# Kernel optimization log

Hardware: AMD Instinct MI355X
Metric: run time of the kernel (lower is better)

The kernel has to match this reference:

```python
import jax, jax.numpy as jnp
import numpy as np

N, MEM_SIZE, MEM_DIM = 65536, 2048, 256

def setup_inputs() -> dict:
    key = jax.random.key(0)
    k1, k2 = jax.random.split(key)
    x = jax.random.normal(k1, (N, MEM_DIM), dtype=jnp.float32)
    # xavier_uniform for memory parameter [memory_size, memory_dim]
    limit = np.sqrt(6.0 / (MEM_SIZE + MEM_DIM)).astype(np.float32)
    memory = jax.random.uniform(k2, (MEM_SIZE, MEM_DIM), dtype=jnp.float32,
                                minval=-limit, maxval=limit)
    return {"x": x, "memory": memory}

def reference(x, memory):
    # scores: [N, memory_size] = x @ memory^T (unscaled)
    scores = jnp.einsum('nd,md->nm', x, memory)
    attention_weights = jax.nn.softmax(scores, axis=-1)
    memory_output = jnp.einsum('nm,md->nd', attention_weights, memory)
    return (memory_output, attention_weights)
```

## Files before the change

### kernel.cpp

```cpp
#include <hip/hip_runtime.h>
#include <hip/hip_bf16.h>
#include <stdint.h>

#define NQ 65536
#define MM 2048
#define DD 256

typedef __bf16 bf16x8 __attribute__((ext_vector_type(8)));
typedef float f32x16 __attribute__((ext_vector_type(16)));
typedef unsigned short u16;
typedef unsigned int u32;
typedef u16 u16x8 __attribute__((ext_vector_type(8)));

typedef __attribute__((address_space(3))) u32 lds_u32;
typedef __attribute__((address_space(1))) u32 glb_u32;

#define GLOAD16(gsrc, ldst)                                                    \
  __builtin_amdgcn_global_load_lds((glb_u32*)(uintptr_t)(gsrc),                \
                                   (lds_u32*)(u32)(uintptr_t)(ldst), 16, 0, 0)

__device__ __forceinline__ u16 f32_to_bf16_rtne(float v) {
  u32 u = __builtin_bit_cast(u32, v);
  u += 0x7FFFu + ((u >> 16) & 1u);
  return (u16)(u >> 16);
}

__global__ __launch_bounds__(256) void mem_convert_kernel(
    const float* __restrict__ memory, u16* __restrict__ memb,
    u16* __restrict__ memTswz) {
  int tid = blockIdx.x * 256 + threadIdx.x;
  u16 b = f32_to_bf16_rtne(memory[tid]);
  memb[tid] = b;
  int m = tid >> 8, d = tid & 255;
  int t = m >> 5, mi = m & 31;
  int c = mi >> 3, e = mi & 7;
  int slot = c ^ ((d >> 1) & 3);
  memTswz[(size_t)t * 8192 + (size_t)(d * 4 + slot) * 8 + e] = b;
}

template <bool STORE_BF16>
__global__ __launch_bounds__(256, 2) void pass1_kernel(
    const float* __restrict__ x, const u16* __restrict__ memb,
    u16* __restrict__ p_e, float* __restrict__ outWf,
    float* __restrict__ sums) {
  __shared__ __align__(16) char stage[2][32768];

  const int tid = threadIdx.x;
  const int wv = tid >> 6;
  const int l = tid & 63;
  const int q5 = l & 31;
  const int h = l >> 5;
  const int qw = blockIdx.x * 128 + wv * 32;

  bf16x8 aq[16];
  {
    const float* xrow = x + (size_t)(qw + q5) * DD;
#pragma unroll
    for (int ks = 0; ks < 16; ++ks) {
      const float4 f0 = *(const float4*)(xrow + ks * 16 + h * 8);
      const float4 f1 = *(const float4*)(xrow + ks * 16 + h * 8 + 4);
      bf16x8 a;
      a[0] = (__bf16)f0.x; a[1] = (__bf16)f0.y;
      a[2] = (__bf16)f0.z; a[3] = (__bf16)f0.w;
      a[4] = (__bf16)f1.x; a[5] = (__bf16)f1.y;
      a[6] = (__bf16)f1.z; a[7] = (__bf16)f1.w;
      aq[ks] = a;
    }
  }

  auto STAGE1 = [&](int mt, char* buf) {
#pragma unroll
    for (int i = 0; i < 8; ++i) {
      const int wc = wv * 8 + i;
      const int row = wc * 2 + h;
      const int csrc = q5 ^ (row & 7);
      GLOAD16(memb + (((size_t)(mt * 64 + row)) << 8) + csrc * 8,
              buf + (wc << 10));
    }
  };

  float part[16];
#pragma unroll
  for (int r = 0; r < 16; ++r) part[r] = 0.f;

  STAGE1(0, stage[0]);
  __syncthreads();
  for (int mt = 0; mt < 32; ++mt) {
    char* cur = stage[mt & 1];
    char* nxt = stage[(mt & 1) ^ 1];
    if (mt + 1 < 32) STAGE1(mt + 1, nxt);
#pragma unroll
    for (int msub = 0; msub < 2; ++msub) {
      const int mrow = msub * 32 + q5;
      const char* bbase = cur + mrow * 512;
      const int sw = mrow & 7;
      f32x16 acc = 0.f;
      __builtin_amdgcn_s_setprio(1);
#pragma unroll
      for (int ks = 0; ks < 16; ++ks) {
        bf16x8 b = *(const bf16x8*)(bbase + (((ks * 2 + h) ^ sw) << 4));
        acc = __builtin_amdgcn_mfma_f32_32x32x16_bf16(aq[ks], b, acc, 0, 0, 0);
      }
      __builtin_amdgcn_s_setprio(0);
      const int tm = mt * 2 + msub;
#pragma unroll
      for (int r = 0; r < 16; ++r) {
        const int qrow = (r & 3) + 8 * (r >> 2) + 4 * h;
        const float e = __expf(acc[r]);
        part[r] += e;
        if (STORE_BF16) {
          p_e[(size_t)(qw + qrow) * MM + tm * 32 + q5] = f32_to_bf16_rtne(e);
        } else {
          outWf[(size_t)(qw + qrow) * MM + tm * 32 + q5] = e;
        }
      }
    }
    __syncthreads();
  }

#pragma unroll
  for (int r = 0; r < 16; ++r) {
    float p = part[r];
    p += __shfl_xor(p, 1, 64);
    p += __shfl_xor(p, 2, 64);
    p += __shfl_xor(p, 4, 64);
    p += __shfl_xor(p, 8, 64);
    p += __shfl_xor(p, 16, 64);
    if (q5 == 0) sums[qw + (r & 3) + 8 * (r >> 2) + 4 * h] = p;
  }
}

template <bool LOAD_BF16>
__global__ __launch_bounds__(256, 2) void pass2_kernel(
    const u16* __restrict__ p_e, const u16* __restrict__ memTswz,
    const float* __restrict__ sums, float* __restrict__ outO,
    float* __restrict__ outW) {
  __shared__ __align__(16) char tstage[2][16384];

  const int tid = threadIdx.x;
  const int wv = tid >> 6;
  const int l = tid & 63;
  const int q5 = l & 31;
  const int h = l >> 5;
  const int qw = blockIdx.x * 128 + wv * 32;

  const float inv_lane = 1.0f / sums[qw + q5];
  float invr[16];
#pragma unroll
  for (int r = 0; r < 16; ++r) {
    invr[r] = __shfl(inv_lane, (r & 3) + 8 * (r >> 2) + 4 * h, 64);
  }

  auto STAGE = [&](int t, char* buf) {
#pragma unroll
    for (int i = 0; i < 4; ++i) {
      const int ci = wv * 4 + i;
      GLOAD16(memTswz + ((size_t)t * 1024 + ci * 64 + l) * 8, buf + (ci << 10));
    }
  };

  f32x16 oacc[8];
#pragma unroll
  for (int i = 0; i < 8; ++i) oacc[i] = 0.f;

  STAGE(0, tstage[0]);
  __syncthreads();
  for (int tm = 0; tm < 64; ++tm) {
    char* cur = tstage[tm & 1];
    char* nxt = tstage[(tm & 1) ^ 1];
    if (tm + 1 < 64) STAGE(tm + 1, nxt);

    bf16x8 pa[2];
    if (LOAD_BF16) {
      const u16* prow = p_e + (size_t)(qw + q5) * MM + tm * 32;
#pragma unroll
      for (int ks2 = 0; ks2 < 2; ++ks2) {
        u16x8 pe = *(const u16x8*)(prow + ks2 * 16 + h * 8);
        pa[ks2] = __builtin_bit_cast(bf16x8, pe);
        float w[8];
#pragma unroll
        for (int j = 0; j < 8; ++j) {
          w[j] = __builtin_bit_cast(float, (u32)pe[j] << 16) * inv_lane;
        }
        float* base =
            outW + (size_t)(qw + q5) * MM + tm * 32 + ks2 * 16 + h * 8;
        *(float4*)base = make_float4(w[0], w[1], w[2], w[3]);
        *(float4*)(base + 4) = make_float4(w[4], w[5], w[6], w[7]);
      }
    } else {
      float* wrow = outW + (size_t)(qw + q5) * MM + tm * 32;
#pragma unroll
      for (int ks2 = 0; ks2 < 2; ++ks2) {
        float4 f0 = *(const float4*)(wrow + ks2 * 16 + h * 8);
        float4 f1 = *(const float4*)(wrow + ks2 * 16 + h * 8 + 4);
        float w0 = f0.x * inv_lane, w1 = f0.y * inv_lane;
        float w2 = f0.z * inv_lane, w3 = f0.w * inv_lane;
        float w4 = f1.x * inv_lane, w5 = f1.y * inv_lane;
        float w6 = f1.z * inv_lane, w7 = f1.w * inv_lane;
        *(float4*)(wrow + ks2 * 16 + h * 8) = make_float4(w0, w1, w2, w3);
        *(float4*)(wrow + ks2 * 16 + h * 8 + 4) = make_float4(w4, w5, w6, w7);
        bf16x8 p;
        p[0] = (__bf16)(w0 * 1.0f); p[1] = (__bf16)w1; p[2] = (__bf16)w2;
        p[3] = (__bf16)w3; p[4] = (__bf16)w4; p[5] = (__bf16)w5;
        p[6] = (__bf16)w6; p[7] = (__bf16)w7;
        pa[ks2] = p;
      }
    }

    __builtin_amdgcn_s_setprio(1);
#pragma unroll
    for (int ks2 = 0; ks2 < 2; ++ks2) {
#pragma unroll
      for (int dsub = 0; dsub < 8; ++dsub) {
        const int d = dsub * 32 + q5;
        const int slot = (2 * ks2 + h) ^ ((d >> 1) & 3);
        bf16x8 b = *(const bf16x8*)(cur + d * 64 + slot * 16);
        oacc[dsub] =
            __builtin_amdgcn_mfma_f32_32x32x16_bf16(pa[ks2], b, oacc[dsub], 0,
                                                    0, 0);
      }
    }
    __builtin_amdgcn_s_setprio(0);
    __syncthreads();
  }

#pragma unroll
  for (int dsub = 0; dsub < 8; ++dsub) {
#pragma unroll
    for (int r = 0; r < 16; ++r) {
      const int qrow = (r & 3) + 8 * (r >> 2) + 4 * h;
      const float scale = LOAD_BF16 ? invr[r] : 1.0f;
      outO[(size_t)(qw + qrow) * DD + dsub * 32 + q5] = oacc[dsub][r] * scale;
    }
  }
}

extern "C" void kernel_launch(void* const* d_in, const int* in_sizes, int n_in,
                              void* d_out, int out_size, void* d_ws,
                              size_t ws_size, hipStream_t stream) {
  const float* x = (const float*)d_in[0];
  const float* memory = (const float*)d_in[1];
  float* outO = (float*)d_out;
  float* outW = outO + (size_t)NQ * DD;

  u16* memb = (u16*)d_ws;
  u16* memTswz = memb + (size_t)MM * DD;
  float* sums = (float*)(memTswz + (size_t)MM * DD);
  u16* p_e = (u16*)(sums + NQ);
  const size_t need = (size_t)MM * DD * 2 * 2 + (size_t)NQ * 4 +
                      (size_t)NQ * MM * 2;

  mem_convert_kernel<<<dim3((MM * DD) / 256), dim3(256), 0, stream>>>(
      memory, memb, memTswz);
  if (ws_size >= need) {
    pass1_kernel<true><<<dim3(NQ / 128), dim3(256), 0, stream>>>(
        x, memb, p_e, outW, sums);
    pass2_kernel<true><<<dim3(NQ / 128), dim3(256), 0, stream>>>(
        p_e, memTswz, sums, outO, outW);
  } else {
    pass1_kernel<false><<<dim3(NQ / 128), dim3(256), 0, stream>>>(
        x, memb, p_e, outW, sums);
    pass2_kernel<false><<<dim3(NQ / 128), dim3(256), 0, stream>>>(
        p_e, memTswz, sums, outO, outW);
  }
}
```

Baseline: 418.5 us.

## Drop LDS staging and read memory operands directly from global in both passes

Removes the double-buffered LDS staging (global_load_lds plus barriers) in both GEMM passes. Each wave now loads its MFMA B operands straight from global/L2, using a plain row-major transposed copy of memory in place of the swizzled tiled layout. This removes barrier synchronisation and the LDS footprint, which could raise occupancy. The cost is that each of the four waves re-fetches the same memory tiles through the cache hierarchy, and the pass2 transposed loads are strided by rows.

Measured after the change: 774.8 us. 85.1% more time.

```diff
diff --git a/kernel.cpp b/kernel.cpp
--- a/kernel.cpp
+++ b/kernel.cpp
@@ -12,13 +12,6 @@
 typedef unsigned int u32;
 typedef u16 u16x8 __attribute__((ext_vector_type(8)));
 
-typedef __attribute__((address_space(3))) u32 lds_u32;
-typedef __attribute__((address_space(1))) u32 glb_u32;
-
-#define GLOAD16(gsrc, ldst)                                                    \
-  __builtin_amdgcn_global_load_lds((glb_u32*)(uintptr_t)(gsrc),                \
-                                   (lds_u32*)(u32)(uintptr_t)(ldst), 16, 0, 0)
-
 __device__ __forceinline__ u16 f32_to_bf16_rtne(float v) {
   u32 u = __builtin_bit_cast(u32, v);
   u += 0x7FFFu + ((u >> 16) & 1u);
@@ -27,15 +20,12 @@
 
 __global__ __launch_bounds__(256) void mem_convert_kernel(
     const float* __restrict__ memory, u16* __restrict__ memb,
-    u16* __restrict__ memTswz) {
+    u16* __restrict__ memT) {
   int tid = blockIdx.x * 256 + threadIdx.x;
   u16 b = f32_to_bf16_rtne(memory[tid]);
   memb[tid] = b;
   int m = tid >> 8, d = tid & 255;
-  int t = m >> 5, mi = m & 31;
-  int c = mi >> 3, e = mi & 7;
-  int slot = c ^ ((d >> 1) & 3);
-  memTswz[(size_t)t * 8192 + (size_t)(d * 4 + slot) * 8 + e] = b;
+  memT[(size_t)d * MM + m] = b;
 }
 
 template <bool STORE_BF16>
@@ -43,8 +33,6 @@
     const float* __restrict__ x, const u16* __restrict__ memb,
     u16* __restrict__ p_e, float* __restrict__ outWf,
     float* __restrict__ sums) {
-  __shared__ __align__(16) char stage[2][32768];
-
   const int tid = threadIdx.x;
   const int wv = tid >> 6;
   const int l = tid & 63;
@@ -68,54 +56,31 @@
     }
   }
 
-  auto STAGE1 = [&](int mt, char* buf) {
-#pragma unroll
-    for (int i = 0; i < 8; ++i) {
-      const int wc = wv * 8 + i;
-      const int row = wc * 2 + h;
-      const int csrc = q5 ^ (row & 7);
-      GLOAD16(memb + (((size_t)(mt * 64 + row)) << 8) + csrc * 8,
-              buf + (wc << 10));
-    }
-  };
-
   float part[16];
 #pragma unroll
   for (int r = 0; r < 16; ++r) part[r] = 0.f;
 
-  STAGE1(0, stage[0]);
-  __syncthreads();
-  for (int mt = 0; mt < 32; ++mt) {
-    char* cur = stage[mt & 1];
-    char* nxt = stage[(mt & 1) ^ 1];
-    if (mt + 1 < 32) STAGE1(mt + 1, nxt);
-#pragma unroll
-    for (int msub = 0; msub < 2; ++msub) {
-      const int mrow = msub * 32 + q5;
-      const char* bbase = cur + mrow * 512;
-      const int sw = mrow & 7;
-      f32x16 acc = 0.f;
-      __builtin_amdgcn_s_setprio(1);
-#pragma unroll
-      for (int ks = 0; ks < 16; ++ks) {
-        bf16x8 b = *(const bf16x8*)(bbase + (((ks * 2 + h) ^ sw) << 4));
-        acc = __builtin_amdgcn_mfma_f32_32x32x16_bf16(aq[ks], b, acc, 0, 0, 0);
-      }
-      __builtin_amdgcn_s_setprio(0);
-      const int tm = mt * 2 + msub;
-#pragma unroll
-      for (int r = 0; r < 16; ++r) {
-        const int qrow = (r & 3) + 8 * (r >> 2) + 4 * h;
-        const float e = __expf(acc[r]);
-        part[r] += e;
-        if (STORE_BF16) {
-          p_e[(size_t)(qw + qrow) * MM + tm * 32 + q5] = f32_to_bf16_rtne(e);
-        } else {
-          outWf[(size_t)(qw + qrow) * MM + tm * 32 + q5] = e;
-        }
-      }
-    }
-    __syncthreads();
+  for (int tm = 0; tm < 64; ++tm) {
+    const u16* brow = memb + (((size_t)(tm * 32 + q5)) << 8) + h * 8;
+    f32x16 acc = 0.f;
+    __builtin_amdgcn_s_setprio(1);
+#pragma unroll
+    for (int ks = 0; ks < 16; ++ks) {
+      bf16x8 b = *(const bf16x8*)(brow + ks * 16);
+      acc = __builtin_amdgcn_mfma_f32_32x32x16_bf16(aq[ks], b, acc, 0, 0, 0);
+    }
+    __builtin_amdgcn_s_setprio(0);
+#pragma unroll
+    for (int r = 0; r < 16; ++r) {
+      const int qrow = (r & 3) + 8 * (r >> 2) + 4 * h;
+      const float e = __expf(acc[r]);
+      part[r] += e;
+      if (STORE_BF16) {
+        p_e[(size_t)(qw + qrow) * MM + tm * 32 + q5] = f32_to_bf16_rtne(e);
+      } else {
+        outWf[(size_t)(qw + qrow) * MM + tm * 32 + q5] = e;
+      }
+    }
   }
 
 #pragma unroll
@@ -132,11 +97,9 @@
 
 template <bool LOAD_BF16>
 __global__ __launch_bounds__(256, 2) void pass2_kernel(
-    const u16* __restrict__ p_e, const u16* __restrict__ memTswz,
+    const u16* __restrict__ p_e, const u16* __restrict__ memT,
     const float* __restrict__ sums, float* __restrict__ outO,
     float* __restrict__ outW) {
-  __shared__ __align__(16) char tstage[2][16384];
-
   const int tid = threadIdx.x;
   const int wv = tid >> 6;
   const int l = tid & 63;
@@ -151,25 +114,11 @@
     invr[r] = __shfl(inv_lane, (r & 3) + 8 * (r >> 2) + 4 * h, 64);
   }
 
-  auto STAGE = [&](int t, char* buf) {
-#pragma unroll
-    for (int i = 0; i < 4; ++i) {
-      const int ci = wv * 4 + i;
-      GLOAD16(memTswz + ((size_t)t * 1024 + ci * 64 + l) * 8, buf + (ci << 10));
-    }
-  };
-
   f32x16 oacc[8];
 #pragma unroll
   for (int i = 0; i < 8; ++i) oacc[i] = 0.f;
 
-  STAGE(0, tstage[0]);
-  __syncthreads();
   for (int tm = 0; tm < 64; ++tm) {
-    char* cur = tstage[tm & 1];
-    char* nxt = tstage[(tm & 1) ^ 1];
-    if (tm + 1 < 64) STAGE(tm + 1, nxt);
-
     bf16x8 pa[2];
     if (LOAD_BF16) {
       const u16* prow = p_e + (size_t)(qw + q5) * MM + tm * 32;
@@ -200,28 +149,27 @@
         *(float4*)(wrow + ks2 * 16 + h * 8) = make_float4(w0, w1, w2, w3);
         *(float4*)(wrow + ks2 * 16 + h * 8 + 4) = make_float4(w4, w5, w6, w7);
         bf16x8 p;
-        p[0] = (__bf16)(w0 * 1.0f); p[1] = (__bf16)w1; p[2] = (__bf16)w2;
+        p[0] = (__bf16)w0; p[1] = (__bf16)w1; p[2] = (__bf16)w2;
         p[3] = (__bf16)w3; p[4] = (__bf16)w4; p[5] = (__bf16)w5;
         p[6] = (__bf16)w6; p[7] = (__bf16)w7;
         pa[ks2] = p;
       }
     }
 
+    const u16* tbase = memT + (size_t)q5 * MM + tm * 32 + h * 8;
     __builtin_amdgcn_s_setprio(1);
 #pragma unroll
     for (int ks2 = 0; ks2 < 2; ++ks2) {
 #pragma unroll
       for (int dsub = 0; dsub < 8; ++dsub) {
-        const int d = dsub * 32 + q5;
-        const int slot = (2 * ks2 + h) ^ ((d >> 1) & 3);
-        bf16x8 b = *(const bf16x8*)(cur + d * 64 + slot * 16);
+        bf16x8 b =
+            *(const bf16x8*)(tbase + (size_t)dsub * 32 * MM + ks2 * 16);
         oacc[dsub] =
             __builtin_amdgcn_mfma_f32_32x32x16_bf16(pa[ks2], b, oacc[dsub], 0,
                                                     0, 0);
       }
     }
     __builtin_amdgcn_s_setprio(0);
-    __syncthreads();
   }
 
 #pragma unroll
@@ -244,23 +192,23 @@
   float* outW = outO + (size_t)NQ * DD;
 
   u16* memb = (u16*)d_ws;
-  u16* memTswz = memb + (size_t)MM * DD;
-  float* sums = (float*)(memTswz + (size_t)MM * DD);
+  u16* memT = memb + (size_t)MM * DD;
+  float* sums = (float*)(memT + (size_t)MM * DD);
   u16* p_e = (u16*)(sums + NQ);
   const size_t need = (size_t)MM * DD * 2 * 2 + (size_t)NQ * 4 +
                       (size_t)NQ * MM * 2;
 
   mem_convert_kernel<<<dim3((MM * DD) / 256), dim3(256), 0, stream>>>(
-      memory, memb, memTswz);
+      memory, memb, memT);
   if (ws_size >= need) {
     pass1_kernel<true><<<dim3(NQ / 128), dim3(256), 0, stream>>>(
         x, memb, p_e, outW, sums);
     pass2_kernel<true><<<dim3(NQ / 128), dim3(256), 0, stream>>>(
-        p_e, memTswz, sums, outO, outW);
+        p_e, memT, sums, outO, outW);
   } else {
     pass1_kernel<false><<<dim3(NQ / 128), dim3(256), 0, stream>>>(
         x, memb, p_e, outW, sums);
     pass2_kernel<false><<<dim3(NQ / 128), dim3(256), 0, stream>>>(
-        p_e, memTswz, sums, outO, outW);
-  }
-}
+        p_e, memT, sums, outO, outW);
+  }
+}
```

## Split work across wave pairs in both passes to raise occupancy

Applied to the files above, without the earlier changes.

Each block now handles 64 queries instead of 128. In pass 1, two waves share a query tile and each computes half of the memory columns; the row sums are combined through LDS. Pass 1 also moves to a single LDS stage buffer with syncs, dropping double buffering. In pass 2, two waves split the output D dimension, which halves the accumulator registers, and only one wave of each pair writes the normalized weights. Launch bounds rise to 4 blocks per CU to hide latency with more resident waves, at the cost of lost load/compute overlap in pass 1 and duplicated p_e reads in pass 2.

Result: slower. 540.9 us (+29.3%).

```diff
diff --git a/kernel.cpp b/kernel.cpp
--- a/kernel.cpp
+++ b/kernel.cpp
@@ -38,19 +38,20 @@
   memTswz[(size_t)t * 8192 + (size_t)(d * 4 + slot) * 8 + e] = b;
 }
 
-template <bool STORE_BF16>
-__global__ __launch_bounds__(256, 2) void pass1_kernel(
+__global__ __launch_bounds__(256, 4) void pass1_kernel(
     const float* __restrict__ x, const u16* __restrict__ memb,
-    u16* __restrict__ p_e, float* __restrict__ outWf,
-    float* __restrict__ sums) {
-  __shared__ __align__(16) char stage[2][32768];
+    u16* __restrict__ p_e, float* __restrict__ sums) {
+  __shared__ __align__(16) char stage[32768];
+  __shared__ float lsum[2][2][32];
 
   const int tid = threadIdx.x;
   const int wv = tid >> 6;
+  const int g = wv >> 1;
+  const int p = wv & 1;
   const int l = tid & 63;
   const int q5 = l & 31;
   const int h = l >> 5;
-  const int qw = blockIdx.x * 128 + wv * 32;
+  const int qw = blockIdx.x * 64 + g * 32;
 
   bf16x8 aq[16];
   {
@@ -68,70 +69,70 @@
     }
   }
 
-  auto STAGE1 = [&](int mt, char* buf) {
+  float part[16];
+#pragma unroll
+  for (int r = 0; r < 16; ++r) part[r] = 0.f;
+
+  for (int t = 0; t < 32; ++t) {
 #pragma unroll
     for (int i = 0; i < 8; ++i) {
       const int wc = wv * 8 + i;
       const int row = wc * 2 + h;
       const int csrc = q5 ^ (row & 7);
-      GLOAD16(memb + (((size_t)(mt * 64 + row)) << 8) + csrc * 8,
-              buf + (wc << 10));
-    }
-  };
-
-  float part[16];
-#pragma unroll
-  for (int r = 0; r < 16; ++r) part[r] = 0.f;
-
-  STAGE1(0, stage[0]);
+      GLOAD16(memb + (((size_t)(t * 64 + row)) << 8) + csrc * 8,
+              stage + (wc << 10));
+    }
+    __syncthreads();
+
+    const int mrow = p * 32 + q5;
+    const char* bbase = stage + mrow * 512;
+    const int sw = mrow & 7;
+    f32x16 acc = 0.f;
+    __builtin_amdgcn_s_setprio(1);
+#pragma unroll
+    for (int ks = 0; ks < 16; ++ks) {
+      bf16x8 b = *(const bf16x8*)(bbase + (((ks * 2 + h) ^ sw) << 4));
+      acc = __builtin_amdgcn_mfma_f32_32x32x16_bf16(aq[ks], b, acc, 0, 0, 0);
+    }
+    __builtin_amdgcn_s_setprio(0);
+    const int tm = t * 2 + p;
+#pragma unroll
+    for (int r = 0; r < 16; ++r) {
+      const int qrow = (r & 3) + 8 * (r >> 2) + 4 * h;
+      const float e = __expf(acc[r]);
+      part[r] += e;
+      p_e[(size_t)(qw + qrow) * MM + tm * 32 + q5] = f32_to_bf16_rtne(e);
+    }
+    __syncthreads();
+  }
+
+#pragma unroll
+  for (int r = 0; r < 16; ++r) {
+    float s = part[r];
+    s += __shfl_xor(s, 1, 64);
+    s += __shfl_xor(s, 2, 64);
+    s += __shfl_xor(s, 4, 64);
+    s += __shfl_xor(s, 8, 64);
+    s += __shfl_xor(s, 16, 64);
+    part[r] = s;
+  }
+  if (q5 == 0) {
+#pragma unroll
+    for (int r = 0; r < 16; ++r) {
+      lsum[g][p][(r & 3) + 8 * (r >> 2) + 4 * h] = part[r];
+    }
+  }
   __syncthreads();
-  for (int mt = 0; mt < 32; ++mt) {
-    char* cur = stage[mt & 1];
-    char* nxt = stage[(mt & 1) ^ 1];
-    if (mt + 1 < 32) STAGE1(mt + 1, nxt);
-#pragma unroll
-    for (int msub = 0; msub < 2; ++msub) {
-      const int mrow = msub * 32 + q5;
-      const char* bbase = cur + mrow * 512;
-      const int sw = mrow & 7;
-      f32x16 acc = 0.f;
-      __builtin_amdgcn_s_setprio(1);
-#pragma unroll
-      for (int ks = 0; ks < 16; ++ks) {
-        bf16x8 b = *(const bf16x8*)(bbase + (((ks * 2 + h) ^ sw) << 4));
-        acc = __builtin_amdgcn_mfma_f32_32x32x16_bf16(aq[ks], b, acc, 0, 0, 0);
-      }
-      __builtin_amdgcn_s_setprio(0);
-      const int tm = mt * 2 + msub;
-#pragma unroll
-      for (int r = 0; r < 16; ++r) {
-        const int qrow = (r & 3) + 8 * (r >> 2) + 4 * h;
-        const float e = __expf(acc[r]);
-        part[r] += e;
-        if (STORE_BF16) {
-          p_e[(size_t)(qw + qrow) * MM + tm * 32 + q5] = f32_to_bf16_rtne(e);
-        } else {
-          outWf[(size_t)(qw + qrow) * MM + tm * 32 + q5] = e;
-        }
-      }
-    }
-    __syncthreads();
-  }
-
-#pragma unroll
-  for (int r = 0; r < 16; ++r) {
-    float p = part[r];
-    p += __shfl_xor(p, 1, 64);
-    p += __shfl_xor(p, 2, 64);
-    p += __shfl_xor(p, 4, 64);
-    p += __shfl_xor(p, 8, 64);
-    p += __shfl_xor(p, 16, 64);
-    if (q5 == 0) sums[qw + (r & 3) + 8 * (r >> 2) + 4 * h] = p;
-  }
-}
-
-template <bool LOAD_BF16>
-__global__ __launch_bounds__(256, 2) void pass2_kernel(
+  if (p == 0 && q5 == 0) {
+#pragma unroll
+    for (int r = 0; r < 16; ++r) {
+      const int qrow = (r & 3) + 8 * (r >> 2) + 4 * h;
+      sums[qw + qrow] = lsum[g][0][qrow] + lsum[g][1][qrow];
+    }
+  }
+}
+
+__global__ __launch_bounds__(256, 4) void pass2_kernel(
     const u16* __restrict__ p_e, const u16* __restrict__ memTswz,
     const float* __restrict__ sums, float* __restrict__ outO,
     float* __restrict__ outW) {
@@ -139,10 +140,12 @@
 
   const int tid = threadIdx.x;
   const int wv = tid >> 6;
+  const int g = wv >> 1;
+  const int dh = wv & 1;
   const int l = tid & 63;
   const int q5 = l & 31;
   const int h = l >> 5;
-  const int qw = blockIdx.x * 128 + wv * 32;
+  const int qw = blockIdx.x * 64 + g * 32;
 
   const float inv_lane = 1.0f / sums[qw + q5];
   float invr[16];
@@ -159,9 +162,9 @@
     }
   };
 
-  f32x16 oacc[8];
-#pragma unroll
-  for (int i = 0; i < 8; ++i) oacc[i] = 0.f;
+  f32x16 oacc[4];
+#pragma unroll
+  for (int i = 0; i < 4; ++i) oacc[i] = 0.f;
 
   STAGE(0, tstage[0]);
   __syncthreads();
@@ -171,12 +174,12 @@
     if (tm + 1 < 64) STAGE(tm + 1, nxt);
 
     bf16x8 pa[2];
-    if (LOAD_BF16) {
-      const u16* prow = p_e + (size_t)(qw + q5) * MM + tm * 32;
-#pragma unroll
-      for (int ks2 = 0; ks2 < 2; ++ks2) {
-        u16x8 pe = *(const u16x8*)(prow + ks2 * 16 + h * 8);
-        pa[ks2] = __builtin_bit_cast(bf16x8, pe);
+    const u16* prow = p_e + (size_t)(qw + q5) * MM + tm * 32;
+#pragma unroll
+    for (int ks2 = 0; ks2 < 2; ++ks2) {
+      u16x8 pe = *(const u16x8*)(prow + ks2 * 16 + h * 8);
+      pa[ks2] = __builtin_bit_cast(bf16x8, pe);
+      if (dh == 0) {
         float w[8];
 #pragma unroll
         for (int j = 0; j < 8; ++j) {
@@ -187,27 +190,160 @@
         *(float4*)base = make_float4(w[0], w[1], w[2], w[3]);
         *(float4*)(base + 4) = make_float4(w[4], w[5], w[6], w[7]);
       }
-    } else {
-      float* wrow = outW + (size_t)(qw + q5) * MM + tm * 32;
-#pragma unroll
-      for (int ks2 = 0; ks2 < 2; ++ks2) {
-        float4 f0 = *(const float4*)(wrow + ks2 * 16 + h * 8);
-        float4 f1 = *(const float4*)(wrow + ks2 * 16 + h * 8 + 4);
-        float w0 = f0.x * inv_lane, w1 = f0.y * inv_lane;
-        float w2 = f0.z * inv_lane, w3 = f0.w * inv_lane;
-        float w4 = f1.x * inv_lane, w5 = f1.y * inv_lane;
-        float w6 = f1.z * inv_lane, w7 = f1.w * inv_lane;
-        *(float4*)(wrow + ks2 * 16 + h * 8) = make_float4(w0, w1, w2, w3);
-        *(float4*)(wrow + ks2 * 16 + h * 8 + 4) = make_float4(w4, w5, w6, w7);
-        bf16x8 p;
-        p[0] = (__bf16)(w0 * 1.0f); p[1] = (__bf16)w1; p[2] = (__bf16)w2;
-        p[3] = (__bf16)w3; p[4] = (__bf16)w4; p[5] = (__bf16)w5;
-        p[6] = (__bf16)w6; p[7] = (__bf16)w7;
-        pa[ks2] = p;
-      }
     }
 
     __builtin_amdgcn_s_setprio(1);
+#pragma unroll
+    for (int ks2 = 0; ks2 < 2; ++ks2) {
+#pragma unroll
+      for (int i = 0; i < 4; ++i) {
+        const int d = (dh * 4 + i) * 32 + q5;
+        const int slot = (2 * ks2 + h) ^ ((d >> 1) & 3);
+        bf16x8 b = *(const bf16x8*)(cur + d * 64 + slot * 16);
+        oacc[i] =
+            __builtin_amdgcn_mfma_f32_32x32x16_bf16(pa[ks2], b, oacc[i], 0, 0,
+                                                    0);
+      }
+    }
+    __builtin_amdgcn_s_setprio(0);
+    __syncthreads();
+  }
+
+#pragma unroll
+  for (int i = 0; i < 4; ++i) {
+#pragma unroll
+    for (int r = 0; r < 16; ++r) {
+      const int qrow = (r & 3) + 8 * (r >> 2) + 4 * h;
+      outO[(size_t)(qw + qrow) * DD + (dh * 4 + i) * 32 + q5] =
+          oacc[i][r] * invr[r];
+    }
+  }
+}
+
+__global__ __launch_bounds__(256, 2) void pass1_fb(
+    const float* __restrict__ x, const u16* __restrict__ memb,
+    float* __restrict__ outWf, float* __restrict__ sums) {
+  __shared__ __align__(16) char stage[2][32768];
+  const int tid = threadIdx.x;
+  const int wv = tid >> 6;
+  const int l = tid & 63;
+  const int q5 = l & 31;
+  const int h = l >> 5;
+  const int qw = blockIdx.x * 128 + wv * 32;
+
+  bf16x8 aq[16];
+  {
+    const float* xrow = x + (size_t)(qw + q5) * DD;
+#pragma unroll
+    for (int ks = 0; ks < 16; ++ks) {
+      const float4 f0 = *(const float4*)(xrow + ks * 16 + h * 8);
+      const float4 f1 = *(const float4*)(xrow + ks * 16 + h * 8 + 4);
+      bf16x8 a;
+      a[0] = (__bf16)f0.x; a[1] = (__bf16)f0.y;
+      a[2] = (__bf16)f0.z; a[3] = (__bf16)f0.w;
+      a[4] = (__bf16)f1.x; a[5] = (__bf16)f1.y;
+      a[6] = (__bf16)f1.z; a[7] = (__bf16)f1.w;
+      aq[ks] = a;
+    }
+  }
+  auto STAGE1 = [&](int mt, char* buf) {
+#pragma unroll
+    for (int i = 0; i < 8; ++i) {
+      const int wc = wv * 8 + i;
+      const int row = wc * 2 + h;
+      const int csrc = q5 ^ (row & 7);
+      GLOAD16(memb + (((size_t)(mt * 64 + row)) << 8) + csrc * 8,
+              buf + (wc << 10));
+    }
+  };
+  float part[16];
+#pragma unroll
+  for (int r = 0; r < 16; ++r) part[r] = 0.f;
+  STAGE1(0, stage[0]);
+  __syncthreads();
+  for (int mt = 0; mt < 32; ++mt) {
+    char* cur = stage[mt & 1];
+    char* nxt = stage[(mt & 1) ^ 1];
+    if (mt + 1 < 32) STAGE1(mt + 1, nxt);
+#pragma unroll
+    for (int msub = 0; msub < 2; ++msub) {
+      const int mrow = msub * 32 + q5;
+      const char* bbase = cur + mrow * 512;
+      const int sw = mrow & 7;
+      f32x16 acc = 0.f;
+#pragma unroll
+      for (int ks = 0; ks < 16; ++ks) {
+        bf16x8 b = *(const bf16x8*)(bbase + (((ks * 2 + h) ^ sw) << 4));
+        acc = __builtin_amdgcn_mfma_f32_32x32x16_bf16(aq[ks], b, acc, 0, 0, 0);
+      }
+      const int tm = mt * 2 + msub;
+#pragma unroll
+      for (int r = 0; r < 16; ++r) {
+        const int qrow = (r & 3) + 8 * (r >> 2) + 4 * h;
+        const float e = __expf(acc[r]);
+        part[r] += e;
+        outWf[(size_t)(qw + qrow) * MM + tm * 32 + q5] = e;
+      }
+    }
+    __syncthreads();
+  }
+#pragma unroll
+  for (int r = 0; r < 16; ++r) {
+    float s = part[r];
+    s += __shfl_xor(s, 1, 64);
+    s += __shfl_xor(s, 2, 64);
+    s += __shfl_xor(s, 4, 64);
+    s += __shfl_xor(s, 8, 64);
+    s += __shfl_xor(s, 16, 64);
+    if (q5 == 0) sums[qw + (r & 3) + 8 * (r >> 2) + 4 * h] = s;
+  }
+}
+
+__global__ __launch_bounds__(256, 2) void pass2_fb(
+    const u16* __restrict__ memTswz, const float* __restrict__ sums,
+    float* __restrict__ outO, float* __restrict__ outW) {
+  __shared__ __align__(16) char tstage[2][16384];
+  const int tid = threadIdx.x;
+  const int wv = tid >> 6;
+  const int l = tid & 63;
+  const int q5 = l & 31;
+  const int h = l >> 5;
+  const int qw = blockIdx.x * 128 + wv * 32;
+  const float inv_lane = 1.0f / sums[qw + q5];
+  auto STAGE = [&](int t, char* buf) {
+#pragma unroll
+    for (int i = 0; i < 4; ++i) {
+      const int ci = wv * 4 + i;
+      GLOAD16(memTswz + ((size_t)t * 1024 + ci * 64 + l) * 8, buf + (ci << 10));
+    }
+  };
+  f32x16 oacc[8];
+#pragma unroll
+  for (int i = 0; i < 8; ++i) oacc[i] = 0.f;
+  STAGE(0, tstage[0]);
+  __syncthreads();
+  for (int tm = 0; tm < 64; ++tm) {
+    char* cur = tstage[tm & 1];
+    char* nxt = tstage[(tm & 1) ^ 1];
+    if (tm + 1 < 64) STAGE(tm + 1, nxt);
+    float* wrow = outW + (size_t)(qw + q5) * MM + tm * 32;
+    bf16x8 pa[2];
+#pragma unroll
+    for (int ks2 = 0; ks2 < 2; ++ks2) {
+      float4 f0 = *(const float4*)(wrow + ks2 * 16 + h * 8);
+      float4 f1 = *(const float4*)(wrow + ks2 * 16 + h * 8 + 4);
+      float w0 = f0.x * inv_lane, w1 = f0.y * inv_lane;
+      float w2 = f0.z * inv_lane, w3 = f0.w * inv_lane;
+      float w4 = f1.x * inv_lane, w5 = f1.y * inv_lane;
+      float w6 = f1.z * inv_lane, w7 = f1.w * inv_lane;
+      *(float4*)(wrow + ks2 * 16 + h * 8) = make_float4(w0, w1, w2, w3);
+      *(float4*)(wrow + ks2 * 16 + h * 8 + 4) = make_float4(w4, w5, w6, w7);
+      bf16x8 p;
+      p[0] = (__bf16)w0; p[1] = (__bf16)w1; p[2] = (__bf16)w2;
+      p[3] = (__bf16)w3; p[4] = (__bf16)w4; p[5] = (__bf16)w5;
+      p[6] = (__bf16)w6; p[7] = (__bf16)w7;
+      pa[ks2] = p;
+    }
 #pragma unroll
     for (int ks2 = 0; ks2 < 2; ++ks2) {
 #pragma unroll
@@ -220,17 +356,14 @@
                                                     0, 0);
       }
     }
-    __builtin_amdgcn_s_setprio(0);
-    __syncthreads();
-  }
-
+    __syncthreads();
+  }
 #pragma unroll
   for (int dsub = 0; dsub < 8; ++dsub) {
 #pragma unroll
     for (int r = 0; r < 16; ++r) {
       const int qrow = (r & 3) + 8 * (r >> 2) + 4 * h;
-      const float scale = LOAD_BF16 ? invr[r] : 1.0f;
-      outO[(size_t)(qw + qrow) * DD + dsub * 32 + q5] = oacc[dsub][r] * scale;
+      outO[(size_t)(qw + qrow) * DD + dsub * 32 + q5] = oacc[dsub][r];
     }
   }
 }
@@ -253,14 +386,12 @@
   mem_convert_kernel<<<dim3((MM * DD) / 256), dim3(256), 0, stream>>>(
       memory, memb, memTswz);
   if (ws_size >= need) {
-    pass1_kernel<true><<<dim3(NQ / 128), dim3(256), 0, stream>>>(
-        x, memb, p_e, outW, sums);
-    pass2_kernel<true><<<dim3(NQ / 128), dim3(256), 0, stream>>>(
-        p_e, memTswz, sums, outO, outW);
+    pass1_kernel<<<dim3(NQ / 64), dim3(256), 0, stream>>>(x, memb, p_e, sums);
+    pass2_kernel<<<dim3(NQ / 64), dim3(256), 0, stream>>>(p_e, memTswz, sums,
+                                                          outO, outW);
   } else {
-    pass1_kernel<false><<<dim3(NQ / 128), dim3(256), 0, stream>>>(
-        x, memb, p_e, outW, sums);
-    pass2_kernel<false><<<dim3(NQ / 128), dim3(256), 0, stream>>>(
-        p_e, memTswz, sums, outO, outW);
-  }
-}
+    pass1_fb<<<dim3(NQ / 128), dim3(256), 0, stream>>>(x, memb, outW, sums);
+    pass2_fb<<<dim3(NQ / 128), dim3(256), 0, stream>>>(memTswz, sums, outO,
+                                                       outW);
+  }
+}
```
